# Performance work log

Hardware: AMD Instinct MI355X
Metric: run time of the kernel (lower is better)

Reference implementation:

```python
import jax, jax.numpy as jnp
import numpy as np

T, B, E, H = 1024, 64, 512, 512


def setup_inputs() -> dict:
    key = jax.random.key(0)
    ks = jax.random.split(key, 13)
    a = 1.0 / np.sqrt(H)
    u = lambda k, shape, lo=-a, hi=a: jax.random.uniform(k, shape, jnp.float32, lo, hi)
    return {
        "embeds": jax.random.normal(ks[0], (T, B, E), jnp.float32),
        "w_gx": u(ks[1], (E, H)), "w_gh": u(ks[2], (H, H)), "bias_g": u(ks[3], (H,)),
        "w_ix": u(ks[4], (E, H)), "w_ih": u(ks[5], (H, H)), "bias_i": u(ks[6], (H,)),
        "w_fx": u(ks[7], (E, H)), "w_fh": u(ks[8], (H, H)), "bias_f": u(ks[9], (H,), 1.0 - a, 1.0 + a),
        "w_ox": u(ks[10], (E, H)), "w_oh": u(ks[11], (H, H)), "bias_o": u(ks[12], (H,)),
    }


def reference(embeds, w_gx, w_gh, bias_g, w_ix, w_ih, bias_i,
              w_fx, w_fh, bias_f, w_ox, w_oh, bias_o):
    # Precompute all input projections in one big batched matmul: [T,B,4H]
    Wx = jnp.concatenate([w_gx, w_ix, w_fx, w_ox], axis=1)            # [E,4H]
    Wh = jnp.concatenate([w_gh, w_ih, w_fh, w_oh], axis=1)            # [H,4H]
    b = jnp.concatenate([bias_g, bias_i, bias_f, bias_o], axis=0)     # [4H]
    x_proj = jnp.einsum("tbe,ef->tbf", embeds, Wx) + b                # [T,B,4H]

    Bsz = embeds.shape[1]
    h0 = jnp.zeros((Bsz, H), embeds.dtype)
    c0 = jnp.zeros((Bsz, H), embeds.dtype)

    def step(carry, xp):
        h, c = carry
        z = xp + h @ Wh                                               # [B,4H]
        g = jnp.tanh(z[:, :H])
        i = jax.nn.sigmoid(z[:, H:2 * H])
        f = jax.nn.sigmoid(z[:, 2 * H:3 * H])
        o = jax.nn.sigmoid(z[:, 3 * H:])
        c_new = g * i + c * f
        h_new = jnp.tanh(c_new) * o
        return (h_new, c_new), h_new

    _, hs = jax.lax.scan(step, (h0, c0), x_proj)
    return hs  # [T,B,H]
```

## Files before the change

kernel.cpp:

```cpp
#include <hip/hip_runtime.h>
#include <stdint.h>
#include <stddef.h>


#define Tn 1024
#define Bn 64
#define Hn 512
#define En 512
#define NGROUP 4
#define NJBLK 32
#define NBLOCK (NGROUP * NJBLK)
#define POISON8 0x7F807F807F807F80ull
#define INIT8   0xAAAAAAAAAAAAAAAAull

using bf16x8 = __attribute__((ext_vector_type(8))) __bf16;
using f32x4  = __attribute__((ext_vector_type(4))) float;
using u16x8  = __attribute__((ext_vector_type(8))) unsigned short;
using u16x4  = __attribute__((ext_vector_type(4))) unsigned short;

__device__ __forceinline__ unsigned short f2bf(float f) {
    unsigned u = __builtin_bit_cast(unsigned, f);
    unsigned r = (u + 0x7FFFu + ((u >> 16) & 1u)) >> 16;
    return (unsigned short)r;
}
__device__ __forceinline__ float bf2f(unsigned short b) {
    unsigned u = ((unsigned)b) << 16;
    return __builtin_bit_cast(float, u);
}

__global__ __launch_bounds__(256, 1) void lstm_persistent(
    const float* __restrict__ embeds,
    const float* __restrict__ wx0, const float* __restrict__ wh0, const float* __restrict__ bs0,
    const float* __restrict__ wx1, const float* __restrict__ wh1, const float* __restrict__ bs1,
    const float* __restrict__ wx2, const float* __restrict__ wh2, const float* __restrict__ bs2,
    const float* __restrict__ wx3, const float* __restrict__ wh3, const float* __restrict__ bs3,
    float* __restrict__ out, void* __restrict__ ws)
{
    __shared__ unsigned short Xhi[16][520];
    __shared__ unsigned short Xlo[16][520];
    __shared__ unsigned short Hl[16][520];
    __shared__ float exch[4][16][17];
    __shared__ unsigned short hstage[16][16];

    const int tid  = threadIdx.x;
    const int wav  = tid >> 6;
    const int lane = tid & 63;
    const int q    = lane >> 4;
    const int n    = lane & 15;

    const int bidx = blockIdx.x;
    const int gid  = (bidx >> 1) & 3;
    const int kid  = ((bidx >> 3) << 1) | (bidx & 1);
    const int b0   = gid * 16;
    const int j0   = kid * 16;

    unsigned long long* gbase = (unsigned long long*)ws + (size_t)gid * 3 * 2048;

    const float* wxp = (wav == 0) ? wx0 : (wav == 1) ? wx1 : (wav == 2) ? wx2 : wx3;
    const float* whp = (wav == 0) ? wh0 : (wav == 1) ? wh1 : (wav == 2) ? wh2 : wh3;
    const float* bsp = (wav == 0) ? bs0 : (wav == 1) ? bs1 : (wav == 2) ? bs2 : bs3;

    bf16x8 WXhi[16], WXlo[16], WHhi[16], WHlo[16];
    const int col = j0 + n;
    #pragma unroll
    for (int kk = 0; kk < 16; ++kk) {
        u16x8 xh, xl, hh, hl;
        #pragma unroll
        for (int i = 0; i < 8; ++i) {
            int k = kk * 32 + q * 8 + i;
            float w  = wxp[(size_t)k * Hn + col];
            unsigned short hi = f2bf(w);
            xh[i] = hi;
            xl[i] = f2bf(w - bf2f(hi));
            w  = whp[(size_t)k * Hn + col];
            hi = f2bf(w);
            hh[i] = hi;
            hl[i] = f2bf(w - bf2f(hi));
        }
        WXhi[kk] = __builtin_bit_cast(bf16x8, xh);
        WXlo[kk] = __builtin_bit_cast(bf16x8, xl);
        WHhi[kk] = __builtin_bit_cast(bf16x8, hh);
        WHlo[kk] = __builtin_bit_cast(bf16x8, hl);
    }
    const float bias_l = bsp[col];
    float c_state = 0.f;
    const int b = tid >> 4, j = tid & 15;

    float4 xpre[8];
    #pragma unroll
    for (int it = 0; it < 8; ++it) {
        int idx = tid + it * 256;
        int r = idx >> 7, c4 = idx & 127;
        xpre[it] = ((const float4*)(embeds + ((size_t)(b0 + r)) * En))[c4];
    }

    for (int t = 1; t <= Tn; ++t) {
        const int tau = t - 1;

        #pragma unroll
        for (int it = 0; it < 8; ++it) {
            int idx = tid + it * 256;
            int r = idx >> 7, c4 = idx & 127;
            float4 v = xpre[it];
            float fs[4] = {v.x, v.y, v.z, v.w};
            u16x4 vh, vl;
            #pragma unroll
            for (int e = 0; e < 4; ++e) {
                unsigned short hb = f2bf(fs[e]);
                vh[e] = hb;
                vl[e] = f2bf(fs[e] - bf2f(hb));
            }
            *(u16x4*)&Xhi[r][c4 * 4] = vh;
            *(u16x4*)&Xlo[r][c4 * 4] = vl;
        }
        __syncthreads();

        unsigned long long hv8[8];
        unsigned long long* src = gbase + (size_t)((t - 1) % 3) * 2048;
        if (t > 1) {
            #pragma unroll
            for (int i = 0; i < 8; ++i)
                hv8[i] = __hip_atomic_load(src + tid + i * 256,
                                           __ATOMIC_RELAXED, __HIP_MEMORY_SCOPE_AGENT);
        }

        if (t < Tn) {
            #pragma unroll
            for (int it = 0; it < 8; ++it) {
                int idx = tid + it * 256;
                int r = idx >> 7, c4 = idx & 127;
                xpre[it] = ((const float4*)(embeds + ((size_t)t * Bn + b0 + r) * En))[c4];
            }
        }

        f32x4 acc, acc2;
        acc[0] = bias_l; acc[1] = bias_l; acc[2] = bias_l; acc[3] = bias_l;
        acc2[0] = 0.f; acc2[1] = 0.f; acc2[2] = 0.f; acc2[3] = 0.f;

        #pragma unroll
        for (int kk = 0; kk < 16; ++kk) {
            bf16x8 ah = __builtin_bit_cast(bf16x8, *(const u16x8*)&Xhi[n][kk * 32 + q * 8]);
            bf16x8 al = __builtin_bit_cast(bf16x8, *(const u16x8*)&Xlo[n][kk * 32 + q * 8]);
            acc  = __builtin_amdgcn_mfma_f32_16x16x32_bf16(ah, WXhi[kk], acc, 0, 0, 0);
            acc2 = __builtin_amdgcn_mfma_f32_16x16x32_bf16(ah, WXlo[kk], acc2, 0, 0, 0);
            acc2 = __builtin_amdgcn_mfma_f32_16x16x32_bf16(al, WXhi[kk], acc2, 0, 0, 0);
        }

        if (t > 1) {
            int bad = 0;
            #pragma unroll
            for (int i = 0; i < 8; ++i)
                bad |= (hv8[i] == POISON8 || hv8[i] == INIT8) ? (1 << i) : 0;
            while (bad) {
                #pragma unroll
                for (int i = 0; i < 8; ++i)
                    if (bad & (1 << i))
                        hv8[i] = __hip_atomic_load(src + tid + i * 256,
                                                   __ATOMIC_RELAXED, __HIP_MEMORY_SCOPE_AGENT);
                int nb = 0;
                #pragma unroll
                for (int i = 0; i < 8; ++i)
                    nb |= (hv8[i] == POISON8 || hv8[i] == INIT8) ? (1 << i) : 0;
                bad = nb;
            }
            #pragma unroll
            for (int i = 0; i < 8; ++i) {
                int idx = tid + i * 256, r = idx >> 7, c8 = idx & 127;
                *(u16x4*)&Hl[r][c8 * 4] = __builtin_bit_cast(u16x4, hv8[i]);
            }
        }

        if (tid < 64) {
            int rr = tid >> 2, cq = tid & 3;
            __hip_atomic_store(gbase + (size_t)((t + 1) % 3) * 2048
                                   + rr * 128 + (j0 >> 2) + cq,
                               (unsigned long long)POISON8,
                               __ATOMIC_RELAXED, __HIP_MEMORY_SCOPE_AGENT);
        }

        if (t > 1) {
            __syncthreads();
            #pragma unroll
            for (int kk = 0; kk < 16; ++kk) {
                bf16x8 a = __builtin_bit_cast(bf16x8, *(const u16x8*)&Hl[n][kk * 32 + q * 8]);
                acc  = __builtin_amdgcn_mfma_f32_16x16x32_bf16(a, WHhi[kk], acc, 0, 0, 0);
                acc2 = __builtin_amdgcn_mfma_f32_16x16x32_bf16(a, WHlo[kk], acc2, 0, 0, 0);
            }
        }

        #pragma unroll
        for (int r = 0; r < 4; ++r) {
            float zv  = acc[r] + acc2[r];
            float arg = (wav == 0) ? -2.f * zv : -zv;
            float s   = __builtin_amdgcn_rcpf(1.f + __expf(arg));
            float act = (wav == 0) ? (2.f * s - 1.f) : s;
            exch[wav][q * 4 + r][n] = act;
        }
        __syncthreads();

        float hv;
        {
            float g  = exch[0][b][j];
            float ig = exch[1][b][j];
            float fg = exch[2][b][j];
            float og = exch[3][b][j];
            c_state = g * ig + c_state * fg;
            float e2 = __expf(-2.f * c_state);
            float th = 2.f * __builtin_amdgcn_rcpf(1.f + e2) - 1.f;
            hv = th * og;
            hstage[b][j] = f2bf(hv);
        }
        __syncthreads();

        if (t < Tn && tid < 64) {
            int rr = tid >> 2, cq = tid & 3;
            unsigned long long qv =
                *(const unsigned long long*)&hstage[rr][cq * 4];
            __hip_atomic_store(gbase + (size_t)(t % 3) * 2048
                                   + rr * 128 + (j0 >> 2) + cq,
                               qv, __ATOMIC_RELAXED, __HIP_MEMORY_SCOPE_AGENT);
        }

        out[((size_t)tau * Bn + b0 + b) * Hn + j0 + j] = hv;
    }
}

extern "C" void kernel_launch(void* const* d_in, const int* in_sizes, int n_in,
                              void* d_out, int out_size, void* d_ws, size_t ws_size,
                              hipStream_t stream) {
    lstm_persistent<<<dim3(NBLOCK), dim3(256), 0, stream>>>(
        (const float*)d_in[0],
        (const float*)d_in[1], (const float*)d_in[2], (const float*)d_in[3],
        (const float*)d_in[4], (const float*)d_in[5], (const float*)d_in[6],
        (const float*)d_in[7], (const float*)d_in[8], (const float*)d_in[9],
        (const float*)d_in[10], (const float*)d_in[11], (const float*)d_in[12],
        (float*)d_out, d_ws);
}
```

Baseline: 3.199 ms.

## Do cell update in one wave, drop staging barrier, issue h loads earlier

The cell-state update and hidden-state publish move into wave 0 alone. Each lane now handles four adjacent columns and writes the packed bf16 h directly to the global exchange buffer, which removes the hstage buffer and one __syncthreads per step. The atomic loads of the previous h are issued before the X conversion so their latency overlaps that work, and the X bf16 split uses native __bf16 casts. In exchange, the elementwise tail is serialized onto one wave while the other three wait, and the exch padding changes to allow float4 reads.

Result: slower. 4.522 ms (+41.4%).

```diff
diff --git a/kernel.cpp b/kernel.cpp
--- a/kernel.cpp
+++ b/kernel.cpp
@@ -39,8 +39,7 @@
     __shared__ unsigned short Xhi[16][520];
     __shared__ unsigned short Xlo[16][520];
     __shared__ unsigned short Hl[16][520];
-    __shared__ float exch[4][16][17];
-    __shared__ unsigned short hstage[16][16];
+    __shared__ float exch[4][16][20];
 
     const int tid  = threadIdx.x;
     const int wav  = tid >> 6;
@@ -83,53 +82,55 @@
         WHlo[kk] = __builtin_bit_cast(bf16x8, hl);
     }
     const float bias_l = bsp[col];
-    float c_state = 0.f;
-    const int b = tid >> 4, j = tid & 15;
+
+    const int pb = lane >> 2, pc = lane & 3;
+    float c4[4] = {0.f, 0.f, 0.f, 0.f};
 
     float4 xpre[8];
     #pragma unroll
     for (int it = 0; it < 8; ++it) {
         int idx = tid + it * 256;
-        int r = idx >> 7, c4 = idx & 127;
-        xpre[it] = ((const float4*)(embeds + ((size_t)(b0 + r)) * En))[c4];
+        int r = idx >> 7, cc = idx & 127;
+        xpre[it] = ((const float4*)(embeds + ((size_t)(b0 + r)) * En))[cc];
     }
 
     for (int t = 1; t <= Tn; ++t) {
         const int tau = t - 1;
 
+        unsigned long long hv8[8];
+        unsigned long long* src = gbase + (size_t)((t - 1) % 3) * 2048;
+        if (t > 1) {
+            #pragma unroll
+            for (int i = 0; i < 8; ++i)
+                hv8[i] = __hip_atomic_load(src + tid + i * 256,
+                                           __ATOMIC_RELAXED, __HIP_MEMORY_SCOPE_AGENT);
+        }
+
         #pragma unroll
         for (int it = 0; it < 8; ++it) {
             int idx = tid + it * 256;
-            int r = idx >> 7, c4 = idx & 127;
+            int r = idx >> 7, cc = idx & 127;
             float4 v = xpre[it];
             float fs[4] = {v.x, v.y, v.z, v.w};
             u16x4 vh, vl;
             #pragma unroll
             for (int e = 0; e < 4; ++e) {
-                unsigned short hb = f2bf(fs[e]);
-                vh[e] = hb;
-                vl[e] = f2bf(fs[e] - bf2f(hb));
-            }
-            *(u16x4*)&Xhi[r][c4 * 4] = vh;
-            *(u16x4*)&Xlo[r][c4 * 4] = vl;
+                __bf16 hb = (__bf16)fs[e];
+                vh[e] = __builtin_bit_cast(unsigned short, hb);
+                vl[e] = __builtin_bit_cast(unsigned short,
+                                           (__bf16)(fs[e] - (float)hb));
+            }
+            *(u16x4*)&Xhi[r][cc * 4] = vh;
+            *(u16x4*)&Xlo[r][cc * 4] = vl;
         }
         __syncthreads();
-
-        unsigned long long hv8[8];
-        unsigned long long* src = gbase + (size_t)((t - 1) % 3) * 2048;
-        if (t > 1) {
-            #pragma unroll
-            for (int i = 0; i < 8; ++i)
-                hv8[i] = __hip_atomic_load(src + tid + i * 256,
-                                           __ATOMIC_RELAXED, __HIP_MEMORY_SCOPE_AGENT);
-        }
 
         if (t < Tn) {
             #pragma unroll
             for (int it = 0; it < 8; ++it) {
                 int idx = tid + it * 256;
-                int r = idx >> 7, c4 = idx & 127;
-                xpre[it] = ((const float4*)(embeds + ((size_t)t * Bn + b0 + r) * En))[c4];
+                int r = idx >> 7, cc = idx & 127;
+                xpre[it] = ((const float4*)(embeds + ((size_t)t * Bn + b0 + r) * En))[cc];
             }
         }
 
@@ -198,30 +199,34 @@
         }
         __syncthreads();
 
-        float hv;
-        {
-            float g  = exch[0][b][j];
-            float ig = exch[1][b][j];
-            float fg = exch[2][b][j];
-            float og = exch[3][b][j];
-            c_state = g * ig + c_state * fg;
-            float e2 = __expf(-2.f * c_state);
-            float th = 2.f * __builtin_amdgcn_rcpf(1.f + e2) - 1.f;
-            hv = th * og;
-            hstage[b][j] = f2bf(hv);
-        }
-        __syncthreads();
-
-        if (t < Tn && tid < 64) {
-            int rr = tid >> 2, cq = tid & 3;
-            unsigned long long qv =
-                *(const unsigned long long*)&hstage[rr][cq * 4];
-            __hip_atomic_store(gbase + (size_t)(t % 3) * 2048
-                                   + rr * 128 + (j0 >> 2) + cq,
-                               qv, __ATOMIC_RELAXED, __HIP_MEMORY_SCOPE_AGENT);
-        }
-
-        out[((size_t)tau * Bn + b0 + b) * Hn + j0 + j] = hv;
+        if (wav == 0) {
+            float4 gv = *(const float4*)&exch[0][pb][pc * 4];
+            float4 iv = *(const float4*)&exch[1][pb][pc * 4];
+            float4 fv = *(const float4*)&exch[2][pb][pc * 4];
+            float4 ov = *(const float4*)&exch[3][pb][pc * 4];
+            float gg[4] = {gv.x, gv.y, gv.z, gv.w};
+            float ii[4] = {iv.x, iv.y, iv.z, iv.w};
+            float ff[4] = {fv.x, fv.y, fv.z, fv.w};
+            float oo[4] = {ov.x, ov.y, ov.z, ov.w};
+            float hv[4];
+            u16x4 pk;
+            #pragma unroll
+            for (int e = 0; e < 4; ++e) {
+                c4[e] = gg[e] * ii[e] + c4[e] * ff[e];
+                float e2 = __expf(-2.f * c4[e]);
+                float th = 2.f * __builtin_amdgcn_rcpf(1.f + e2) - 1.f;
+                hv[e] = th * oo[e];
+                pk[e] = f2bf(hv[e]);
+            }
+            if (t < Tn) {
+                __hip_atomic_store(gbase + (size_t)(t % 3) * 2048
+                                       + pb * 128 + (j0 >> 2) + pc,
+                                   __builtin_bit_cast(unsigned long long, pk),
+                                   __ATOMIC_RELAXED, __HIP_MEMORY_SCOPE_AGENT);
+            }
+            float4 o4; o4.x = hv[0]; o4.y = hv[1]; o4.z = hv[2]; o4.w = hv[3];
+            *(float4*)(out + ((size_t)tau * Bn + b0 + pb) * Hn + j0 + pc * 4) = o4;
+        }
     }
 }
 
```
